# Kernel tuning notes

Measured on AMD Instinct MI355X. Metric: run time of the kernel, lower is better.

The kernel has to match this reference:

```python
import jax, jax.numpy as jnp
import numpy as np

NEG_SLOPE = 0.2

def setup_inputs() -> dict:
    key = jax.random.key(0)
    ks = jax.random.split(key, 10)
    N, E, D = 50000, 1250000, 64
    indices = jax.random.randint(ks[0], (2, E), 0, N, dtype=jnp.int64)
    features = jax.random.normal(ks[1], (N, D), dtype=jnp.float32)
    edge_types = jax.random.randint(ks[2], (E,), 0, 4, dtype=jnp.int64)
    s = 1.0 / np.sqrt(D)
    return {
        "indices": indices,
        "features": features,
        "edge_types": edge_types,
        "num_nodes": N,
        "W1_w": jax.random.uniform(ks[3], (D, D), jnp.float32, -s, s),
        "W1_b": jax.random.uniform(ks[4], (D,), jnp.float32, -s, s),
        "W2_w": jax.random.uniform(ks[5], (D, D), jnp.float32, -s, s),
        "W2_b": jax.random.uniform(ks[6], (D,), jnp.float32, -s, s),
        "W_att_w": jax.random.uniform(ks[7], (D, D), jnp.float32, -s, s),
        "W_att_b": jax.random.uniform(ks[8], (D,), jnp.float32, -s, s),
        "a": jax.random.normal(ks[9], (2 * D, 1), jnp.float32) * np.sqrt(2.0 / (2 * D + 1)),
    }


def reference(indices, features, edge_types, num_nodes, W1_w, W1_b, W2_w, W2_b, W_att_w, W_att_b, a):
    src, dst = indices[0], indices[1]
    D = W_att_w.shape[0]
    scaling = 1.0 / jnp.sqrt(jnp.float32(D))

    # Attention transform; cat([h_src, h_dst]) @ a == h_src@a1 + h_dst@a2
    h_trans = features @ W_att_w.T + W_att_b              # (N, D)
    a1, a2 = a[:D, 0], a[D:, 0]
    s_src = h_trans @ a1                                  # (N,)
    s_dst = h_trans @ a2                                  # (N,)
    e_raw = s_src[src] + s_dst[dst]                       # (E,)

    bias = jnp.where(edge_types == 0, 5.0, 0.0)           # ingredient bias
    e = jax.nn.leaky_relu((e_raw + bias) * scaling, NEG_SLOPE).astype(jnp.float32)

    # segment softmax over destination nodes (max is detached in original)
    max_score = jax.lax.stop_gradient(jax.ops.segment_max(e, dst, num_segments=num_nodes))
    max_score = jnp.where(jnp.isfinite(max_score), max_score, -1e9)
    exp_e = jnp.exp(e - max_score[dst])                   # (E,)
    denom = jax.ops.segment_sum(exp_e, dst, num_segments=num_nodes)
    alpha = exp_e / (denom[dst] + 1e-9)                   # (E,)

    # message passing
    h_msg = features @ W1_w.T + W1_b                      # (N, D)
    weighted = h_msg[src] * alpha[:, None]                # (E, D)
    h_neigh = jax.ops.segment_sum(weighted, dst, num_segments=num_nodes)  # (N, D)

    h_self = features                                     # in_dim == out_dim
    sum_h = h_self + h_neigh
    prod_h = h_self * h_neigh
    h_out = jax.nn.leaky_relu(sum_h + prod_h @ W2_w.T + W2_b, NEG_SLOPE)
    return h_out
```

## Files before the change

### kernel.cpp

```cpp
#include <hip/hip_runtime.h>
#include <math.h>

#define DD 64
#define WSTR 68
#define NEG_SLOPE 0.2f
#define SCALING 0.125f
#define CAP 64

__device__ __forceinline__ float lrelu(float x) { return x >= 0.0f ? x : NEG_SLOPE * x; }

__device__ __forceinline__ unsigned bf16_rne(float f) {
    unsigned u = __float_as_uint(f);
    u += 0x7FFFu + ((u >> 16) & 1u);
    return u >> 16;
}

__device__ __forceinline__ float bfly_sum64(float v) {
    #pragma unroll
    for (int off = 1; off < 64; off <<= 1) v += __shfl_xor(v, off);
    return v;
}

__global__ __launch_bounds__(256) void k_node1(
        const float* __restrict__ feat, const float* __restrict__ Watt,
        const float* __restrict__ Wattb, const float* __restrict__ a,
        float* __restrict__ s_src, float* __restrict__ s_dst,
        unsigned* __restrict__ feat16, int* __restrict__ cnt, int N) {
    __shared__ float v1s[DD], v2s[DD], csh[2];
    int t = threadIdx.x;
    if (t < 64) {
        float s1 = 0.f, s2 = 0.f;
        for (int d = 0; d < DD; ++d) {
            float w = Watt[d * DD + t];
            s1 = fmaf(w, a[d], s1);
            s2 = fmaf(w, a[DD + d], s2);
        }
        v1s[t] = s1; v2s[t] = s2;
        float b = Wattb[t];
        float p1 = bfly_sum64(b * a[t]);
        float p2 = bfly_sum64(b * a[DD + t]);
        if (t == 0) { csh[0] = p1; csh[1] = p2; }
    }
    __syncthreads();
    int lane = t & 63, wslot = t >> 6;
    float v1l = v1s[lane], v2l = v2s[lane], c1 = csh[0], c2 = csh[1];
    int n0 = (blockIdx.x * 4 + wslot) * 4;
    if (n0 >= N) return;

    float fd[4], p1[4], p2[4];
    #pragma unroll
    for (int i = 0; i < 4; ++i) {
        int n = n0 + i;
        fd[i] = (n < N) ? feat[n * DD + lane] : 0.f;
        p1[i] = fd[i] * v1l;
        p2[i] = fd[i] * v2l;
    }
    #pragma unroll
    for (int off = 1; off < 64; off <<= 1) {
        #pragma unroll
        for (int i = 0; i < 4; ++i) {
            p1[i] += __shfl_xor(p1[i], off);
            p2[i] += __shfl_xor(p2[i], off);
        }
    }
    #pragma unroll
    for (int i = 0; i < 4; ++i) {
        int n = n0 + i;
        unsigned me = bf16_rne(fd[i]);
        unsigned pair = me | (__shfl_down(me, 1) << 16);
        unsigned v = __shfl(pair, 2 * lane);
        if (n < N) {
            if (lane < 32) feat16[n * 32 + lane] = v;
            if (lane == 0) { s_src[n] = p1[i] + c1; s_dst[n] = p2[i] + c2; cnt[n] = 0; }
        }
    }
}

__global__ void k_bucket(const int* __restrict__ src, const int* __restrict__ dst,
                         const int* __restrict__ et,
                         const float* __restrict__ s_src, const float* __restrict__ s_dst,
                         int* __restrict__ cnt, unsigned* __restrict__ wpack, int E) {
    int p = blockIdx.x & 7;
    int q = blockIdx.x >> 3;
    int stride = (gridDim.x >> 3) * blockDim.x;
    for (int i = q * blockDim.x + threadIdx.x; i < E; i += stride) {
        int d = dst[i];
        if ((d & 7) != p) continue;
        int s = src[i];
        float e = s_src[s] + s_dst[d] + (et[i] == 0 ? 5.0f : 0.0f);
        float w = __expf(lrelu(e * SCALING));
        int slot = atomicAdd(&cnt[d], 1);
        if (slot > CAP - 1) slot = CAP - 1;
        wpack[(d << 6) + slot] = (bf16_rne(w) << 16) | (unsigned)s;
    }
}

__global__ __launch_bounds__(256) void k_gather(
        const float* __restrict__ feat, const unsigned* __restrict__ feat16,
        const float* __restrict__ W1, const float* __restrict__ W1b,
        const float* __restrict__ W2, const float* __restrict__ W2b,
        const int* __restrict__ cnt, const unsigned* __restrict__ wpack,
        float* __restrict__ out, int N) {
    __shared__ float W1p[DD * WSTR], W2p[DD * WSTR];
    __shared__ float plds[4][DD];
    int t = threadIdx.x;
    for (int i = t; i < DD * DD; i += 256) {
        int d = i >> 6, k = i & 63;
        W1p[d * WSTR + k] = W1[i];
        W2p[d * WSTR + k] = W2[i];
    }
    __syncthreads();
    int lane = t & 63, wslot = t >> 6;
    int c = lane & 31, h = lane >> 5;
    float b1l = W1b[lane], b2l = W2b[lane];
    const float4* wrow1 = (const float4*)&W1p[lane * WSTR];
    const float4* wrow2 = (const float4*)&W2p[lane * WSTR];
    float* pl = plds[wslot];
    int wv = blockIdx.x * 4 + wslot;
    int nw = gridDim.x * 4;
    for (int n = wv; n < N; n += nw) {
        int m = cnt[n]; if (m > CAP) m = CAP;
        unsigned u = wpack[(n << 6) + lane];
        if (lane >= m) u = 0;

        float ax = 0.f, ay = 0.f, bx = 0.f, by = 0.f, l = 0.f;
        int tt = 0;
        for (; tt + 8 <= m; tt += 8) {
            unsigned e0 = __shfl(u, tt + h);
            unsigned e1 = __shfl(u, tt + 2 + h);
            unsigned e2 = __shfl(u, tt + 4 + h);
            unsigned e3 = __shfl(u, tt + 6 + h);
            unsigned v0 = feat16[(e0 & 0xFFFFu) * 32 + c];
            unsigned v1 = feat16[(e1 & 0xFFFFu) * 32 + c];
            unsigned v2 = feat16[(e2 & 0xFFFFu) * 32 + c];
            unsigned v3 = feat16[(e3 & 0xFFFFu) * 32 + c];
            float w0 = __uint_as_float(e0 & 0xFFFF0000u);
            float w1 = __uint_as_float(e1 & 0xFFFF0000u);
            float w2 = __uint_as_float(e2 & 0xFFFF0000u);
            float w3 = __uint_as_float(e3 & 0xFFFF0000u);
            ax = fmaf(w0, __uint_as_float(v0 << 16), ax);
            ay = fmaf(w0, __uint_as_float(v0 & 0xFFFF0000u), ay);
            bx = fmaf(w1, __uint_as_float(v1 << 16), bx);
            by = fmaf(w1, __uint_as_float(v1 & 0xFFFF0000u), by);
            ax = fmaf(w2, __uint_as_float(v2 << 16), ax);
            ay = fmaf(w2, __uint_as_float(v2 & 0xFFFF0000u), ay);
            bx = fmaf(w3, __uint_as_float(v3 << 16), bx);
            by = fmaf(w3, __uint_as_float(v3 & 0xFFFF0000u), by);
            l += (w0 + w1) + (w2 + w3);
        }
        for (; tt < m; tt += 2) {
            unsigned e0 = __shfl(u, tt + h);
            unsigned v0 = feat16[(e0 & 0xFFFFu) * 32 + c];
            float w0 = __uint_as_float(e0 & 0xFFFF0000u);
            ax = fmaf(w0, __uint_as_float(v0 << 16), ax);
            ay = fmaf(w0, __uint_as_float(v0 & 0xFFFF0000u), ay);
            l += w0;
        }
        ax += bx; ay += by;
        ax += __shfl_xor(ax, 32);
        ay += __shfl_xor(ay, 32);
        l  += __shfl_xor(l, 32);
        float inv = 1.f / (l + 1e-9f);

        if (h == 0) { pl[2 * c] = ax; pl[2 * c + 1] = ay; }
        float acc1 = l * b1l;
        #pragma unroll
        for (int k4 = 0; k4 < 16; ++k4) {
            float4 w = wrow1[k4];
            float4 g = *(const float4*)&pl[k4 * 4];
            acc1 = fmaf(g.x, w.x, acc1);
            acc1 = fmaf(g.y, w.y, acc1);
            acc1 = fmaf(g.z, w.z, acc1);
            acc1 = fmaf(g.w, w.w, acc1);
        }
        float hn = acc1 * inv;
        float fd = feat[n * DD + lane];
        pl[lane] = fd * hn;
        float acc2 = b2l;
        #pragma unroll
        for (int k4 = 0; k4 < 16; ++k4) {
            float4 w = wrow2[k4];
            float4 pk = *(const float4*)&pl[k4 * 4];
            acc2 = fmaf(pk.x, w.x, acc2);
            acc2 = fmaf(pk.y, w.y, acc2);
            acc2 = fmaf(pk.z, w.z, acc2);
            acc2 = fmaf(pk.w, w.w, acc2);
        }
        out[n * DD + lane] = lrelu(fd + hn + acc2);
    }
}

extern "C" void kernel_launch(void* const* d_in, const int* in_sizes, int n_in,
                              void* d_out, int out_size, void* d_ws, size_t ws_size,
                              hipStream_t stream) {
    const int*   indices = (const int*)d_in[0];
    const float* feat    = (const float*)d_in[1];
    const int*   etype   = (const int*)d_in[2];
    const float* W1      = (const float*)d_in[4];
    const float* W1b     = (const float*)d_in[5];
    const float* W2      = (const float*)d_in[6];
    const float* W2b     = (const float*)d_in[7];
    const float* Watt    = (const float*)d_in[8];
    const float* Wattb   = (const float*)d_in[9];
    const float* a       = (const float*)d_in[10];

    const int E = in_sizes[2];
    const int N = in_sizes[1] / DD;
    const int* src = indices;
    const int* dst = indices + E;

    float* ws = (float*)d_ws;
    float*    s_src  = ws;
    float*    s_dst  = s_src + N;
    int*      cnt    = (int*)(s_dst + N);
    unsigned* feat16 = (unsigned*)(cnt + N);
    unsigned* wpack  = feat16 + (size_t)N * 32;

    k_node1<<<(N + 15) / 16, 256, 0, stream>>>(feat, Watt, Wattb, a,
                                               s_src, s_dst, feat16, cnt, N);
    k_bucket<<<2048, 256, 0, stream>>>(src, dst, etype, s_src, s_dst,
                                       cnt, wpack, E);
    k_gather<<<1024, 256, 0, stream>>>(feat, feat16, W1, W1b, W2, W2b,
                                       cnt, wpack, (float*)d_out, N);
}
```

Baseline: 208.8 us.

## Split edge bucketing into partition pass and scatter pass

The bucketing kernel previously had each of 8 partition groups scan the whole edge list and skip edges whose destination did not fall in its partition, reading the edge arrays eight times. It now runs as two kernels. The first computes each edge weight once and writes packed records into 8 per-partition lists, staged in shared memory so each block needs only one global atomic per partition. The second scatters each partition's list into the per-node slots. This cuts the repeated reads of the edge arrays but adds an intermediate array of 8-byte records, one extra launch, and more workspace, and the second pass has to re-read that intermediate array.

Result: slower. 264.1 us (+26.5%).

```diff
diff --git a/kernel.cpp b/kernel.cpp
--- a/kernel.cpp
+++ b/kernel.cpp
@@ -6,6 +6,8 @@
 #define NEG_SLOPE 0.2f
 #define SCALING 0.125f
 #define CAP 64
+#define PART 8
+#define CAPB 128
 
 __device__ __forceinline__ float lrelu(float x) { return x >= 0.0f ? x : NEG_SLOPE * x; }
 
@@ -25,9 +27,11 @@
         const float* __restrict__ feat, const float* __restrict__ Watt,
         const float* __restrict__ Wattb, const float* __restrict__ a,
         float* __restrict__ s_src, float* __restrict__ s_dst,
-        unsigned* __restrict__ feat16, int* __restrict__ cnt, int N) {
+        unsigned* __restrict__ feat16, int* __restrict__ cnt,
+        int* __restrict__ gcur, int N) {
     __shared__ float v1s[DD], v2s[DD], csh[2];
     int t = threadIdx.x;
+    if (blockIdx.x == 0 && t < PART) gcur[t] = 0;
     if (t < 64) {
         float s1 = 0.f, s2 = 0.f;
         for (int d = 0; d < DD; ++d) {
@@ -76,22 +80,57 @@
     }
 }
 
-__global__ void k_bucket(const int* __restrict__ src, const int* __restrict__ dst,
-                         const int* __restrict__ et,
-                         const float* __restrict__ s_src, const float* __restrict__ s_dst,
-                         int* __restrict__ cnt, unsigned* __restrict__ wpack, int E) {
+__global__ __launch_bounds__(256) void k_bucketA(
+        const int* __restrict__ src, const int* __restrict__ dst,
+        const int* __restrict__ et,
+        const float* __restrict__ s_src, const float* __restrict__ s_dst,
+        int* __restrict__ gcur, uint2* __restrict__ plist, int pcap, int E) {
+    __shared__ uint2 buf[PART][CAPB];
+    __shared__ int cnt8[PART], base8[PART];
+    int t = threadIdx.x;
+    for (long long cbase = (long long)blockIdx.x * 256; cbase < E;
+         cbase += (long long)gridDim.x * 256) {
+        if (t < PART) cnt8[t] = 0;
+        __syncthreads();
+        int i = (int)cbase + t;
+        if (i < E) {
+            int d = dst[i], s = src[i];
+            float e = s_src[s] + s_dst[d] + (et[i] == 0 ? 5.0f : 0.0f);
+            float w = __expf(lrelu(e * SCALING));
+            uint2 rec = make_uint2((bf16_rne(w) << 16) | (unsigned)s, (unsigned)d);
+            int p = d & 7;
+            int pos = atomicAdd(&cnt8[p], 1);
+            if (pos < CAPB) buf[p][pos] = rec;
+            else { int g = atomicAdd(&gcur[p], 1); plist[p * pcap + g] = rec; }
+        }
+        __syncthreads();
+        if (t < PART) {
+            int nr = cnt8[t]; if (nr > CAPB) nr = CAPB;
+            base8[t] = atomicAdd(&gcur[t], nr);
+        }
+        __syncthreads();
+        #pragma unroll
+        for (int pp = 0; pp < PART; ++pp) {
+            int nr = cnt8[pp]; if (nr > CAPB) nr = CAPB;
+            int gb = base8[pp];
+            for (int j = t; j < nr; j += 256) plist[pp * pcap + gb + j] = buf[pp][j];
+        }
+        __syncthreads();
+    }
+}
+
+__global__ __launch_bounds__(256) void k_bucketB(
+        const int* __restrict__ gcur, const uint2* __restrict__ plist, int pcap,
+        int* __restrict__ cnt, unsigned* __restrict__ wpack) {
     int p = blockIdx.x & 7;
-    int q = blockIdx.x >> 3;
-    int stride = (gridDim.x >> 3) * blockDim.x;
-    for (int i = q * blockDim.x + threadIdx.x; i < E; i += stride) {
-        int d = dst[i];
-        if ((d & 7) != p) continue;
-        int s = src[i];
-        float e = s_src[s] + s_dst[d] + (et[i] == 0 ? 5.0f : 0.0f);
-        float w = __expf(lrelu(e * SCALING));
+    int M = gcur[p];
+    int stride = (gridDim.x >> 3) * 256;
+    for (int j = (blockIdx.x >> 3) * 256 + threadIdx.x; j < M; j += stride) {
+        uint2 r = plist[p * pcap + j];
+        int d = (int)r.y;
         int slot = atomicAdd(&cnt[d], 1);
         if (slot > CAP - 1) slot = CAP - 1;
-        wpack[(d << 6) + slot] = (bf16_rne(w) << 16) | (unsigned)s;
+        wpack[(d << 6) + slot] = r.x;
     }
 }
 
@@ -208,18 +247,22 @@
     const int N = in_sizes[1] / DD;
     const int* src = indices;
     const int* dst = indices + E;
+    const int pcap = E / PART + 8192;
 
     float* ws = (float*)d_ws;
     float*    s_src  = ws;
     float*    s_dst  = s_src + N;
     int*      cnt    = (int*)(s_dst + N);
-    unsigned* feat16 = (unsigned*)(cnt + N);
+    int*      gcur   = cnt + N;
+    unsigned* feat16 = (unsigned*)(gcur + 16);
     unsigned* wpack  = feat16 + (size_t)N * 32;
+    uint2*    plist  = (uint2*)(wpack + (size_t)N * 64);
 
     k_node1<<<(N + 15) / 16, 256, 0, stream>>>(feat, Watt, Wattb, a,
-                                               s_src, s_dst, feat16, cnt, N);
-    k_bucket<<<2048, 256, 0, stream>>>(src, dst, etype, s_src, s_dst,
-                                       cnt, wpack, E);
+                                               s_src, s_dst, feat16, cnt, gcur, N);
+    k_bucketA<<<2048, 256, 0, stream>>>(src, dst, etype, s_src, s_dst,
+                                        gcur, plist, pcap, E);
+    k_bucketB<<<2048, 256, 0, stream>>>(gcur, plist, pcap, cnt, wpack);
     k_gather<<<1024, 256, 0, stream>>>(feat, feat16, W1, W1b, W2, W2b,
                                        cnt, wpack, (float*)d_out, N);
 }
```
